# Performance work log

Measured on AMD Instinct MI355X. Metric: run time of the kernel, lower is better.

The kernel has to match this reference:

```python
import jax, jax.numpy as jnp
import numpy as np

D_DIM, H_DIM, W_DIM = 8, 16, 16
HIDDEN, HEAD = 256, 32
NUM_HEADS = HIDDEN // HEAD


def _rel_indices(D, H, W):
    # 3D relative coordinate indices into the bias table, shape (N, N) each.
    coords = np.stack(np.meshgrid(np.arange(D), np.arange(H), np.arange(W), indexing='ij'),
                      axis=-1).reshape(-1, 3)
    rel = coords[:, None, :] - coords[None, :, :]
    rel[:, :, 0] += D - 1
    rel[:, :, 1] += H - 1
    rel[:, :, 2] += W - 1
    return jnp.asarray(rel[:, :, 0]), jnp.asarray(rel[:, :, 1]), jnp.asarray(rel[:, :, 2])


def setup_inputs() -> dict:
    key = jax.random.key(0)
    ks = jax.random.split(key, 6)
    B = 4
    x = jax.random.normal(ks[0], (B, D_DIM, H_DIM, W_DIM, HIDDEN), dtype=jnp.float32)
    s = 1.0 / np.sqrt(HIDDEN)
    Wq = jax.random.normal(ks[1], (HIDDEN, HIDDEN), dtype=jnp.float32) * s
    Wk = jax.random.normal(ks[2], (HIDDEN, HIDDEN), dtype=jnp.float32) * s
    Wv = jax.random.normal(ks[3], (HIDDEN, HIDDEN), dtype=jnp.float32) * s
    Wo = jax.random.normal(ks[4], (HIDDEN, HIDDEN), dtype=jnp.float32) * s
    bias_table = jax.random.normal(ks[5], (NUM_HEADS, 2 * D_DIM - 1, 2 * H_DIM - 1, 2 * W_DIM - 1),
                                   dtype=jnp.float32) * 0.02
    return {"x": x, "Wq": Wq, "Wk": Wk, "Wv": Wv, "Wo": Wo, "bias_table": bias_table}


def reference(x, Wq, Wk, Wv, Wo, bias_table):
    B, D, H, W, C = x.shape
    N = D * H * W
    rd, rh, rw = _rel_indices(D, H, W)
    # gathered relative-position bias: (num_heads, N, N)
    bias = bias_table[:, rd, rh, rw]

    xf = x.reshape(B, N, C)
    q = (xf @ Wq).reshape(B, N, NUM_HEADS, HEAD).transpose(0, 2, 1, 3)  # b h n d
    k = (xf @ Wk).reshape(B, N, NUM_HEADS, HEAD).transpose(0, 2, 1, 3)
    v = (xf @ Wv).reshape(B, N, NUM_HEADS, HEAD).transpose(0, 2, 1, 3)

    scores = jnp.einsum('bhnd,bhmd->bhnm', q, k) / jnp.sqrt(jnp.float32(HEAD))
    scores = scores + bias[None]  # broadcast over batch
    attn = jax.nn.softmax(scores, axis=-1)
    out = jnp.einsum('bhnm,bhmd->bhnd', attn, v)
    out = out.transpose(0, 2, 1, 3).reshape(B, N, HIDDEN) @ Wo
    return out.reshape(B, D, H, W, HIDDEN)
```

## Files before the change

kernel.cpp:

```cpp
#include <hip/hip_runtime.h>
#include <math.h>

#define HIDDEN 256
#define NHEADS 8
#define HEAD 32
#define NTOK 2048
#define NBIAS 115320
#define HTAB 14415

typedef __attribute__((ext_vector_type(8))) __bf16 bf16x8;
typedef __attribute__((ext_vector_type(4))) float f32x4;
typedef __attribute__((ext_vector_type(16))) float f32x16;
typedef __attribute__((ext_vector_type(4))) unsigned uint32x4;

static __device__ __forceinline__ f32x4 mfma16(bf16x8 a, bf16x8 b, f32x4 c) {
    return __builtin_amdgcn_mfma_f32_16x16x32_bf16(a, b, c, 0, 0, 0);
}
static __device__ __forceinline__ f32x16 mfma32(bf16x8 a, bf16x8 b, f32x16 c) {
    return __builtin_amdgcn_mfma_f32_32x32x16_bf16(a, b, c, 0, 0, 0);
}
static __device__ __forceinline__ float fexp2(float x) {
#if __has_builtin(__builtin_amdgcn_exp2f)
    return __builtin_amdgcn_exp2f(x);
#else
    return exp2f(x);
#endif
}
static __device__ __forceinline__ unsigned pkbf16(float a, float b) {
    unsigned short ua = __builtin_bit_cast(unsigned short, (__bf16)a);
    unsigned short ub = __builtin_bit_cast(unsigned short, (__bf16)b);
    return (unsigned)ua | ((unsigned)ub << 16);
}

__global__ void k_cvt_x(const float* __restrict__ x, __bf16* __restrict__ xb) {
    int i = (blockIdx.x * blockDim.x + threadIdx.x) * 4;
    float4 v = *(const float4*)(x + i);
    xb[i + 0] = (__bf16)v.x;
    xb[i + 1] = (__bf16)v.y;
    xb[i + 2] = (__bf16)v.z;
    xb[i + 3] = (__bf16)v.w;
}

__global__ void k_cvt_w(const float* __restrict__ w0, const float* __restrict__ w1,
                        const float* __restrict__ w2, const float* __restrict__ w3,
                        __bf16* __restrict__ t0, __bf16* __restrict__ t1,
                        __bf16* __restrict__ t2, __bf16* __restrict__ t3) {
    int wsel = blockIdx.x >> 8;
    int i = (blockIdx.x & 255) * 256 + threadIdx.x;
    const float* w = (wsel == 0) ? w0 : (wsel == 1) ? w1 : (wsel == 2) ? w2 : w3;
    __bf16* t = (wsel == 0) ? t0 : (wsel == 1) ? t1 : (wsel == 2) ? t2 : t3;
    int n = i >> 8, k = i & 255;
    t[i] = (__bf16)w[k * 256 + n];
}

__global__ void k_cvt_biasq(const float* __restrict__ bias, float4* __restrict__ btq) {
    int i = blockIdx.x * 256 + threadIdx.x;
    if (i >= NBIAS) return;
    int head = i / HTAB;
    int off = i - head * HTAB;
    int b0 = head * HTAB;
    const float L2E = 1.4426950408889634f;
    int i3 = off + 3 > HTAB - 1 ? HTAB - 1 : off + 3;
    int i2 = off + 2 > HTAB - 1 ? HTAB - 1 : off + 2;
    int i1 = off + 1 > HTAB - 1 ? HTAB - 1 : off + 1;
    btq[i] = make_float4(bias[b0 + i3] * L2E, bias[b0 + i2] * L2E,
                         bias[b0 + i1] * L2E, bias[b0 + off] * L2E);
}

__global__ __launch_bounds__(256) void k_qkv(const __bf16* __restrict__ xb,
                                             const __bf16* __restrict__ wqT,
                                             const __bf16* __restrict__ wkT,
                                             const __bf16* __restrict__ wvT,
                                             __bf16* __restrict__ qb,
                                             __bf16* __restrict__ kb,
                                             __bf16* __restrict__ vb) {
    int wid = blockIdx.x * 4 + (threadIdx.x >> 6);
    int lane = threadIdx.x & 63;
    int ng = wid % 12, mt = wid / 12;
    int lm = lane & 15, lg = lane >> 4, lk = lg * 8;
    int which = ng >> 2;
    int nc0 = (ng & 3) * 64;
    const __bf16* wT = (which == 0) ? wqT : (which == 1) ? wkT : wvT;

    f32x4 acc[4][4];
#pragma unroll
    for (int m = 0; m < 4; ++m)
#pragma unroll
        for (int n = 0; n < 4; ++n) acc[m][n] = (f32x4){0.f, 0.f, 0.f, 0.f};

    const __bf16* arow = xb + (size_t)(mt * 64 + lm) * 256 + lk;
    const __bf16* brow = wT + (size_t)(nc0 + lm) * 256 + lk;
#pragma unroll
    for (int kk = 0; kk < 8; ++kk) {
        bf16x8 a[4], b[4];
#pragma unroll
        for (int m = 0; m < 4; ++m) a[m] = *(const bf16x8*)(arow + (size_t)m * 16 * 256 + kk * 32);
#pragma unroll
        for (int n = 0; n < 4; ++n) b[n] = *(const bf16x8*)(brow + (size_t)n * 16 * 256 + kk * 32);
#pragma unroll
        for (int m = 0; m < 4; ++m)
#pragma unroll
            for (int n = 0; n < 4; ++n) acc[m][n] = mfma16(a[m], b[n], acc[m][n]);
    }
    const float QS = 0.17677669529663687f * 1.4426950408889634f;
#pragma unroll
    for (int m = 0; m < 4; ++m) {
#pragma unroll
        for (int n = 0; n < 4; ++n) {
            int col = nc0 + n * 16 + lm;
            int h = col >> 5, d = col & 31;
#pragma unroll
            for (int r = 0; r < 4; ++r) {
                int row = mt * 64 + m * 16 + lg * 4 + r;
                int b_ = row >> 11, tr = row & 2047;
                size_t bh = (size_t)(b_ * 8 + h) * 65536;
                if (which == 0) {
                    qb[bh + (size_t)tr * 32 + d] = (__bf16)(acc[m][n][r] * QS);
                } else if (which == 1) {
                    size_t idx = ((size_t)(tr >> 5) * 128 + (d >> 4) * 64 + ((d >> 3) & 1) * 32 + (tr & 31)) * 8 + (d & 7);
                    kb[bh + idx] = (__bf16)acc[m][n][r];
                } else {
                    size_t idx = ((size_t)(tr >> 5) * 256 + ((tr >> 3) & 3) * 64 + ((tr >> 2) & 1) * 32 + d) * 4 + (tr & 3);
                    vb[bh + idx] = (__bf16)acc[m][n][r];
                }
            }
        }
    }
}

__global__ __launch_bounds__(256) void k_attn(const __bf16* __restrict__ qb,
                                              const __bf16* __restrict__ kb,
                                              const __bf16* __restrict__ vb,
                                              const float4* __restrict__ btqall,
                                              __bf16* __restrict__ attn) {
    int i = blockIdx.x;
    int bh = (i & 7) + ((i >> 9) << 3);
    int qs = (i >> 3) & 63;
    int b_ = bh >> 3, h = bh & 7;
    int w = threadIdx.x >> 6;
    int lane = threadIdx.x & 63;
    int lq = lane & 31;
    int hf = lane >> 5;
    int q0 = qs * 32;

    const __bf16* qbase = qb + (size_t)bh * NTOK * 32;
    const __bf16* kbase = kb + (size_t)bh * NTOK * 32;
    const __bf16* vbase = vb + (size_t)bh * NTOK * 32;
    const float4* btq = btqall + h * HTAB;

    bf16x8 qf0 = *(const bf16x8*)(qbase + (size_t)(q0 + lq) * 32 + hf * 8);
    bf16x8 qf1 = *(const bf16x8*)(qbase + (size_t)(q0 + lq) * 32 + 16 + hf * 8);

    int qg = q0 + lq;
    int qidx4 = (qg >> 8) * 961 + ((qg >> 4) & 15) * 31 + (qg & 15) + 7207 - 4 * hf;

    f32x16 Oacc, Lacc;
#pragma unroll
    for (int j = 0; j < 16; ++j) { Oacc[j] = 0.f; Lacc[j] = 0.f; }

    bf16x8 ones;
#pragma unroll
    for (int j = 0; j < 8; ++j) ones[j] = (__bf16)1.0f;

    f32x4 cb0, cb1, cb2, cb3;
    bf16x8 ck0, ck1;
    {
        int t0 = w * 512;
        int tt = t0 >> 5;
        int c00 = (t0 >> 8) * 961 + ((t0 >> 4) & 15) * 31;
        int jb = qidx4 - c00;
        cb0 = *(const f32x4*)&btq[jb - 3];
        cb1 = *(const f32x4*)&btq[jb - 11];
        cb2 = *(const f32x4*)&btq[jb - 34];
        cb3 = *(const f32x4*)&btq[jb - 42];
        const __bf16* kt = kbase + ((size_t)tt * 128 + lane) * 8;
        ck0 = *(const bf16x8*)(kt);
        ck1 = *(const bf16x8*)(kt + 512);
    }

#pragma unroll
    for (int it = 0; it < 16; ++it) {
        int t0 = w * 512 + it * 32;
        int tt = t0 >> 5;

        f32x4 nb0, nb1, nb2, nb3;
        bf16x8 nk0, nk1;
        if (it < 15) {
            int t1 = t0 + 32;
            int c01 = (t1 >> 8) * 961 + ((t1 >> 4) & 15) * 31;
            int jb1 = qidx4 - c01;
            nb0 = *(const f32x4*)&btq[jb1 - 3];
            nb1 = *(const f32x4*)&btq[jb1 - 11];
            nb2 = *(const f32x4*)&btq[jb1 - 34];
            nb3 = *(const f32x4*)&btq[jb1 - 42];
            const __bf16* kt1 = kbase + ((size_t)(tt + 1) * 128 + lane) * 8;
            nk0 = *(const bf16x8*)(kt1);
            nk1 = *(const bf16x8*)(kt1 + 512);
        }

        const __bf16* vt = vbase + ((size_t)tt * 256 + lane) * 4;
        uint2 va  = *(const uint2*)(vt);
        uint2 vbq = *(const uint2*)(vt + 256);
        uint2 vc  = *(const uint2*)(vt + 512);
        uint2 vd  = *(const uint2*)(vt + 768);
        uint32x4 vw0 = {va.x, va.y, vbq.x, vbq.y};
        uint32x4 vw1 = {vc.x, vc.y, vd.x, vd.y};
        bf16x8 vf0 = __builtin_bit_cast(bf16x8, vw0);
        bf16x8 vf1 = __builtin_bit_cast(bf16x8, vw1);

        f32x16 S;
        S[0]  = cb0[0]; S[1]  = cb0[1]; S[2]  = cb0[2]; S[3]  = cb0[3];
        S[4]  = cb1[0]; S[5]  = cb1[1]; S[6]  = cb1[2]; S[7]  = cb1[3];
        S[8]  = cb2[0]; S[9]  = cb2[1]; S[10] = cb2[2]; S[11] = cb2[3];
        S[12] = cb3[0]; S[13] = cb3[1]; S[14] = cb3[2]; S[15] = cb3[3];
        S = mfma32(ck0, qf0, S);
        S = mfma32(ck1, qf1, S);

        unsigned W0 = pkbf16(fexp2(S[0]),  fexp2(S[1]));
        unsigned W1 = pkbf16(fexp2(S[2]),  fexp2(S[3]));
        unsigned W2 = pkbf16(fexp2(S[4]),  fexp2(S[5]));
        unsigned W3 = pkbf16(fexp2(S[6]),  fexp2(S[7]));
        unsigned W4 = pkbf16(fexp2(S[8]),  fexp2(S[9]));
        unsigned W5 = pkbf16(fexp2(S[10]), fexp2(S[11]));
        unsigned W6 = pkbf16(fexp2(S[12]), fexp2(S[13]));
        unsigned W7 = pkbf16(fexp2(S[14]), fexp2(S[15]));
        uint32x4 pw0 = {W0, W1, W2, W3};
        uint32x4 pw1 = {W4, W5, W6, W7};
        bf16x8 pf0 = __builtin_bit_cast(bf16x8, pw0);
        bf16x8 pf1 = __builtin_bit_cast(bf16x8, pw1);

        Oacc = mfma32(vf0, pf0, Oacc);
        Oacc = mfma32(vf1, pf1, Oacc);
        Lacc = mfma32(ones, pf0, Lacc);
        Lacc = mfma32(ones, pf1, Lacc);

        if (it < 15) {
            cb0 = nb0; cb1 = nb1; cb2 = nb2; cb3 = nb3;
            ck0 = nk0; ck1 = nk1;
        }
    }

    __shared__ float part[4][64][17];
#pragma unroll
    for (int j = 0; j < 4; ++j) {
        float4 t;
        t.x = Oacc[4 * j]; t.y = Oacc[4 * j + 1]; t.z = Oacc[4 * j + 2]; t.w = Oacc[4 * j + 3];
        *(float4*)&part[w][lane][4 * j] = t;
    }
    part[w][lane][16] = Lacc[0];
    __syncthreads();

    float4 o = {0.f, 0.f, 0.f, 0.f};
    float ls = 0.f;
#pragma unroll
    for (int sw = 0; sw < 4; ++sw) {
        float4 t = *(const float4*)&part[sw][lane][4 * w];
        o.x += t.x; o.y += t.y; o.z += t.z; o.w += t.w;
        ls += part[sw][lane][16];
    }
    float inv = 1.0f / ls;
    unsigned lo = pkbf16(o.x * inv, o.y * inv);
    unsigned hi = pkbf16(o.z * inv, o.w * inv);
    size_t base = ((size_t)b_ * NTOK + q0 + lq) * 256 + h * 32 + 8 * w + 4 * hf;
    *(uint2*)(attn + base) = make_uint2(lo, hi);
}

__global__ __launch_bounds__(256) void k_out(const __bf16* __restrict__ attn,
                                             const __bf16* __restrict__ woT,
                                             float* __restrict__ out) {
    int wid = blockIdx.x * 4 + (threadIdx.x >> 6);
    int lane = threadIdx.x & 63;
    int ng = wid & 3, mt = wid >> 2;
    int lm = lane & 15, lg = lane >> 4, lk = lg * 8;
    int nc0 = ng * 64;

    f32x4 acc[4][4];
#pragma unroll
    for (int m = 0; m < 4; ++m)
#pragma unroll
        for (int n = 0; n < 4; ++n) acc[m][n] = (f32x4){0.f, 0.f, 0.f, 0.f};

    const __bf16* arow = attn + (size_t)(mt * 64 + lm) * 256 + lk;
    const __bf16* brow = woT + (size_t)(nc0 + lm) * 256 + lk;
#pragma unroll
    for (int kk = 0; kk < 8; ++kk) {
        bf16x8 a[4], b[4];
#pragma unroll
        for (int m = 0; m < 4; ++m) a[m] = *(const bf16x8*)(arow + (size_t)m * 16 * 256 + kk * 32);
#pragma unroll
        for (int n = 0; n < 4; ++n) b[n] = *(const bf16x8*)(brow + (size_t)n * 16 * 256 + kk * 32);
#pragma unroll
        for (int m = 0; m < 4; ++m)
#pragma unroll
            for (int n = 0; n < 4; ++n) acc[m][n] = mfma16(a[m], b[n], acc[m][n]);
    }
#pragma unroll
    for (int m = 0; m < 4; ++m) {
#pragma unroll
        for (int n = 0; n < 4; ++n) {
            int col = nc0 + n * 16 + lm;
#pragma unroll
            for (int r = 0; r < 4; ++r) {
                int row = mt * 64 + m * 16 + lg * 4 + r;
                out[(size_t)row * 256 + col] = acc[m][n][r];
            }
        }
    }
}

extern "C" void kernel_launch(void* const* d_in, const int* in_sizes, int n_in,
                              void* d_out, int out_size, void* d_ws, size_t ws_size,
                              hipStream_t stream) {
    const float* x    = (const float*)d_in[0];
    const float* Wq   = (const float*)d_in[1];
    const float* Wk   = (const float*)d_in[2];
    const float* Wv   = (const float*)d_in[3];
    const float* Wo   = (const float*)d_in[4];
    const float* bias = (const float*)d_in[5];
    float* out = (float*)d_out;

    __bf16* ws  = (__bf16*)d_ws;
    __bf16* xb  = ws;
    __bf16* wqT = xb  + 2097152;
    __bf16* wkT = wqT + 65536;
    __bf16* wvT = wkT + 65536;
    __bf16* woT = wvT + 65536;
    __bf16* qb  = woT + 65536;
    __bf16* kb  = qb  + 2097152;
    __bf16* vb  = kb  + 2097152;
    float4* btq = (float4*)(vb + 2097152);
    __bf16* att = xb;

    k_cvt_x<<<2048, 256, 0, stream>>>(x, xb);
    k_cvt_w<<<1024, 256, 0, stream>>>(Wq, Wk, Wv, Wo, wqT, wkT, wvT, woT);
    k_cvt_biasq<<<(NBIAS + 255) / 256, 256, 0, stream>>>(bias, btq);
    k_qkv<<<384, 256, 0, stream>>>(xb, wqT, wkT, wvT, qb, kb, vb);
    k_attn<<<2048, 256, 0, stream>>>(qb, kb, vb, btq, att);
    k_out<<<128, 256, 0, stream>>>(att, woT, out);
}
```

Measured before the change: 90.92 us.

## Stage per-block relative bias window in LDS and drop bias preprocessing kernel

Removes the separate kernel that expanded the bias table into a float4 table pre-scaled by log2(e). Each attention block now loads the bias window it needs for its query tile (8x17x33 floats) directly from the raw table into shared memory, scaling it on the fly. The inner loop then reads the bias from LDS instead of prefetching float4 values from global memory. This saves one launch and its global traffic, at the cost of a per-block prologue with integer divisions, an extra barrier, a larger shared allocation that is reused for the reduction buffer, and LDS reads in the hot loop.

```diff
diff --git a/kernel.cpp b/kernel.cpp
--- a/kernel.cpp
+++ b/kernel.cpp
@@ -51,20 +51,6 @@
     __bf16* t = (wsel == 0) ? t0 : (wsel == 1) ? t1 : (wsel == 2) ? t2 : t3;
     int n = i >> 8, k = i & 255;
     t[i] = (__bf16)w[k * 256 + n];
-}
-
-__global__ void k_cvt_biasq(const float* __restrict__ bias, float4* __restrict__ btq) {
-    int i = blockIdx.x * 256 + threadIdx.x;
-    if (i >= NBIAS) return;
-    int head = i / HTAB;
-    int off = i - head * HTAB;
-    int b0 = head * HTAB;
-    const float L2E = 1.4426950408889634f;
-    int i3 = off + 3 > HTAB - 1 ? HTAB - 1 : off + 3;
-    int i2 = off + 2 > HTAB - 1 ? HTAB - 1 : off + 2;
-    int i1 = off + 1 > HTAB - 1 ? HTAB - 1 : off + 1;
-    btq[i] = make_float4(bias[b0 + i3] * L2E, bias[b0 + i2] * L2E,
-                         bias[b0 + i1] * L2E, bias[b0 + off] * L2E);
 }
 
 __global__ __launch_bounds__(256) void k_qkv(const __bf16* __restrict__ xb,
@@ -131,7 +117,7 @@
 __global__ __launch_bounds__(256) void k_attn(const __bf16* __restrict__ qb,
                                               const __bf16* __restrict__ kb,
                                               const __bf16* __restrict__ vb,
-                                              const float4* __restrict__ btqall,
+                                              const float* __restrict__ bias,
                                               __bf16* __restrict__ attn) {
     int i = blockIdx.x;
     int bh = (i & 7) + ((i >> 9) << 3);
@@ -143,16 +129,28 @@
     int hf = lane >> 5;
     int q0 = qs * 32;
 
+    __shared__ float smem[4488];
+
+    {
+        int qd = q0 >> 8, qh0 = (q0 >> 4) & 15;
+        const float* bt = bias + h * HTAB;
+        for (int t = threadIdx.x; t < 4488; t += 256) {
+            int dd = t / 561, rem = t - dd * 561;
+            int hh = rem / 33, ww = rem - hh * 33;
+            int dw = 30 - ww; if (dw < 0) dw = 0;
+            smem[t] = bt[(qd + dd) * 961 + (qh0 + hh) * 31 + dw] * 1.4426950408889634f;
+        }
+    }
+    __syncthreads();
+
     const __bf16* qbase = qb + (size_t)bh * NTOK * 32;
     const __bf16* kbase = kb + (size_t)bh * NTOK * 32;
     const __bf16* vbase = vb + (size_t)bh * NTOK * 32;
-    const float4* btq = btqall + h * HTAB;
 
     bf16x8 qf0 = *(const bf16x8*)(qbase + (size_t)(q0 + lq) * 32 + hf * 8);
     bf16x8 qf1 = *(const bf16x8*)(qbase + (size_t)(q0 + lq) * 32 + 16 + hf * 8);
 
-    int qg = q0 + lq;
-    int qidx4 = (qg >> 8) * 961 + ((qg >> 4) & 15) * 31 + (qg & 15) + 7207 - 4 * hf;
+    int lbase = (lq >> 4) * 33 + 15 - (lq & 15) + 4 * hf;
 
     f32x16 Oacc, Lacc;
 #pragma unroll
@@ -162,18 +160,9 @@
 #pragma unroll
     for (int j = 0; j < 8; ++j) ones[j] = (__bf16)1.0f;
 
-    f32x4 cb0, cb1, cb2, cb3;
     bf16x8 ck0, ck1;
     {
-        int t0 = w * 512;
-        int tt = t0 >> 5;
-        int c00 = (t0 >> 8) * 961 + ((t0 >> 4) & 15) * 31;
-        int jb = qidx4 - c00;
-        cb0 = *(const f32x4*)&btq[jb - 3];
-        cb1 = *(const f32x4*)&btq[jb - 11];
-        cb2 = *(const f32x4*)&btq[jb - 34];
-        cb3 = *(const f32x4*)&btq[jb - 42];
-        const __bf16* kt = kbase + ((size_t)tt * 128 + lane) * 8;
+        const __bf16* kt = kbase + ((size_t)(w * 16) * 128 + lane) * 8;
         ck0 = *(const bf16x8*)(kt);
         ck1 = *(const bf16x8*)(kt + 512);
     }
@@ -183,16 +172,8 @@
         int t0 = w * 512 + it * 32;
         int tt = t0 >> 5;
 
-        f32x4 nb0, nb1, nb2, nb3;
         bf16x8 nk0, nk1;
         if (it < 15) {
-            int t1 = t0 + 32;
-            int c01 = (t1 >> 8) * 961 + ((t1 >> 4) & 15) * 31;
-            int jb1 = qidx4 - c01;
-            nb0 = *(const f32x4*)&btq[jb1 - 3];
-            nb1 = *(const f32x4*)&btq[jb1 - 11];
-            nb2 = *(const f32x4*)&btq[jb1 - 34];
-            nb3 = *(const f32x4*)&btq[jb1 - 42];
             const __bf16* kt1 = kbase + ((size_t)(tt + 1) * 128 + lane) * 8;
             nk0 = *(const bf16x8*)(kt1);
             nk1 = *(const bf16x8*)(kt1 + 512);
@@ -208,11 +189,16 @@
         bf16x8 vf0 = __builtin_bit_cast(bf16x8, vw0);
         bf16x8 vf1 = __builtin_bit_cast(bf16x8, vw1);
 
+        int kd = t0 >> 8, kh0 = (t0 >> 4) & 15;
+        int a0 = (7 - kd) * 561 + (15 - kh0) * 33 + lbase;
         f32x16 S;
-        S[0]  = cb0[0]; S[1]  = cb0[1]; S[2]  = cb0[2]; S[3]  = cb0[3];
-        S[4]  = cb1[0]; S[5]  = cb1[1]; S[6]  = cb1[2]; S[7]  = cb1[3];
-        S[8]  = cb2[0]; S[9]  = cb2[1]; S[10] = cb2[2]; S[11] = cb2[3];
-        S[12] = cb3[0]; S[13] = cb3[1]; S[14] = cb3[2]; S[15] = cb3[3];
+#pragma unroll
+        for (int r = 0; r < 4; ++r) {
+            S[r]      = smem[a0 + r];
+            S[4 + r]  = smem[a0 + 8 + r];
+            S[8 + r]  = smem[a0 - 33 + r];
+            S[12 + r] = smem[a0 - 25 + r];
+        }
         S = mfma32(ck0, qf0, S);
         S = mfma32(ck1, qf1, S);
 
@@ -234,13 +220,11 @@
         Lacc = mfma32(ones, pf0, Lacc);
         Lacc = mfma32(ones, pf1, Lacc);
 
-        if (it < 15) {
-            cb0 = nb0; cb1 = nb1; cb2 = nb2; cb3 = nb3;
-            ck0 = nk0; ck1 = nk1;
-        }
-    }
-
-    __shared__ float part[4][64][17];
+        if (it < 15) { ck0 = nk0; ck1 = nk1; }
+    }
+
+    __syncthreads();
+    float (*part)[64][17] = (float (*)[64][17])smem;
 #pragma unroll
     for (int j = 0; j < 4; ++j) {
         float4 t;
@@ -328,13 +312,11 @@
     __bf16* qb  = woT + 65536;
     __bf16* kb  = qb  + 2097152;
     __bf16* vb  = kb  + 2097152;
-    float4* btq = (float4*)(vb + 2097152);
     __bf16* att = xb;
 
     k_cvt_x<<<2048, 256, 0, stream>>>(x, xb);
     k_cvt_w<<<1024, 256, 0, stream>>>(Wq, Wk, Wv, Wo, wqT, wkT, wvT, woT);
-    k_cvt_biasq<<<(NBIAS + 255) / 256, 256, 0, stream>>>(bias, btq);
     k_qkv<<<384, 256, 0, stream>>>(xb, wqT, wkT, wvT, qb, kb, vb);
-    k_attn<<<2048, 256, 0, stream>>>(qb, kb, vb, btq, att);
+    k_attn<<<2048, 256, 0, stream>>>(qb, kb, vb, bias, att);
     k_out<<<128, 256, 0, stream>>>(att, woT, out);
 }
```

After: 86.95 us. 1.05x faster.
